# Performance work log

Measured on AMD Instinct MI355X. Metric: run time of the kernel, lower is better.

## Reference

```python
import jax, jax.numpy as jnp
import numpy as np

L, B, S, H, NH, DH, I, MAXP, NL = 4, 8, 512, 1024, 32, 32, 4096, 512, 20
EPS = 1e-12


def setup_inputs() -> dict:
    key = jax.random.key(0)
    ks = jax.random.split(key, 12)
    sc = 0.02
    w = lambda k, shape: jax.random.normal(k, shape, jnp.float32) * sc
    p = {}
    p['hidden_states'] = jax.random.normal(ks[0], (B, S, H), jnp.float32)
    p['attention_mask'] = jnp.ones((B, S), jnp.float32)
    p['Wq'] = w(ks[1], (L, H, H)); p['bq'] = jnp.zeros((L, H), jnp.float32)
    p['Wk'] = w(ks[2], (L, H, H)); p['bk'] = jnp.zeros((L, H), jnp.float32)
    p['Wv'] = w(ks[3], (L, H, H)); p['bv'] = jnp.zeros((L, H), jnp.float32)
    p['Wo'] = w(ks[4], (L, H, H)); p['bo'] = jnp.zeros((L, H), jnp.float32)
    p['ln1_g'] = jnp.ones((L, H), jnp.float32); p['ln1_b'] = jnp.zeros((L, H), jnp.float32)
    p['W1'] = w(ks[5], (L, H, I)); p['b1'] = jnp.zeros((L, I), jnp.float32)
    p['W2'] = w(ks[6], (L, I, H)); p['b2'] = jnp.zeros((L, H), jnp.float32)
    p['ln2_g'] = jnp.ones((L, H), jnp.float32); p['ln2_b'] = jnp.zeros((L, H), jnp.float32)
    p['rel_emb'] = w(ks[7], (L, 2 * MAXP - 1, DH))
    p['pool_W'] = w(ks[8], (3 * H, H)); p['pool_b'] = jnp.zeros((H,), jnp.float32)
    p['pool_ln_g'] = jnp.ones((H,), jnp.float32); p['pool_ln_b'] = jnp.zeros((H,), jnp.float32)
    p['cls_W'] = w(ks[9], (H, NL)); p['cls_b'] = jnp.zeros((NL,), jnp.float32)
    return p


def _ln(x, g, b):
    mu = jnp.mean(x, -1, keepdims=True)
    var = jnp.mean(jnp.square(x - mu), -1, keepdims=True)
    return (x - mu) * jax.lax.rsqrt(var + EPS) * g + b


def reference(hidden_states, attention_mask, Wq, bq, Wk, bk, Wv, bv, Wo, bo,
              ln1_g, ln1_b, W1, b1, W2, b2, ln2_g, ln2_b, rel_emb,
              pool_W, pool_b, pool_ln_g, pool_ln_b, cls_W, cls_b):
    b, s, h = hidden_states.shape
    # extended additive attention mask (0 -> -1e9)
    mask_add = (1.0 - attention_mask)[:, None, None, :] * -1e9
    pos = jnp.arange(s)
    rel_idx = pos[:, None] - pos[None, :] + MAXP - 1  # [s, s] in [0, 2*MAXP-2]
    x = hidden_states
    for l in range(L):
        heads = lambda t: t.reshape(b, s, NH, DH).transpose(0, 2, 1, 3)
        q = heads(x @ Wq[l] + bq[l])
        k = heads(x @ Wk[l] + bk[l])
        v = heads(x @ Wv[l] + bv[l])
        # learned relative-position bias; note head_size == num_heads by construction
        rel = rel_emb[l][rel_idx].transpose(2, 0, 1)  # [DH==NH, s, s]
        scores = jnp.einsum('bhqd,bhkd->bhqk', q, k) + rel[None]
        scores = scores / np.float32(np.sqrt(DH)) + mask_add
        probs = jax.nn.softmax(scores, axis=-1)
        ctx = jnp.einsum('bhqk,bhkd->bhqd', probs, v).transpose(0, 2, 1, 3).reshape(b, s, h)
        x = _ln(ctx @ Wo[l] + bo[l] + x, ln1_g[l], ln1_b[l])
        inner = jax.nn.gelu(x @ W1[l] + b1[l], approximate=False) @ W2[l] + b2[l]
        x = _ln(x + inner, ln2_g[l], ln2_b[l])
    # AdvancedPooling: mean + max + first token
    m = attention_mask[..., None]
    mean_pool = jnp.sum(x * m, axis=1) / jnp.sum(attention_mask, axis=1, keepdims=True)
    max_pool = jnp.max(x + (1.0 - m) * -1e9, axis=1)
    pooled = jnp.concatenate([mean_pool, max_pool, x[:, 0]], axis=-1)
    pooled = _ln(pooled @ pool_W + pool_b, pool_ln_g, pool_ln_b)
    return pooled @ cls_W + cls_b
```

## Files before the change

### kernel.cpp

```cpp
#include <hip/hip_runtime.h>
#include <math.h>

typedef __attribute__((ext_vector_type(8))) _Float16 f16x8;
typedef __attribute__((ext_vector_type(4))) float f32x4;

__device__ __forceinline__ ushort f2h(float x) {
  union { _Float16 h; ushort u; } c;
  c.h = (_Float16)x;
  return c.u;
}
__device__ __forceinline__ void gl_lds16(const ushort* g, ushort* l) {
  __builtin_amdgcn_global_load_lds(
      (const __attribute__((address_space(1))) unsigned int*)g,
      (__attribute__((address_space(3))) unsigned int*)l, 16, 0, 0);
}
__device__ __forceinline__ f32x4 mfma16(f16x8 a, f16x8 b, f32x4 c) {
  return __builtin_amdgcn_mfma_f32_16x16x32_f16(a, b, c, 0, 0, 0);
}

__device__ __forceinline__ float block_reduce_sum(float v, float* sb) {
#pragma unroll
  for (int o = 32; o > 0; o >>= 1) v += __shfl_down(v, o, 64);
  const int t = threadIdx.x;
  if ((t & 63) == 0) sb[t >> 6] = v;
  __syncthreads();
  v = sb[0] + sb[1] + sb[2] + sb[3];
  __syncthreads();
  return v;
}

__global__ __launch_bounds__(256) void acast(const float* __restrict__ X,
                                             ushort* __restrict__ H, int n4) {
  const int i = blockIdx.x * 256 + threadIdx.x;
  if (i >= n4) return;
  const float4 x = ((const float4*)X)[i];
  ushort4 h;
  h.x = f2h(x.x); h.y = f2h(x.y); h.z = f2h(x.z); h.w = f2h(x.w);
  ((ushort4*)H)[i] = h;
}

__global__ __launch_bounds__(256) void concat3(const float* __restrict__ a,
                                               const float* __restrict__ b,
                                               const float* __restrict__ c,
                                               float* __restrict__ o) {
  const int i = blockIdx.x * 256 + threadIdx.x;
  o[i] = i < 1024 ? a[i] : (i < 2048 ? b[i - 1024] : c[i - 2048]);
}

__global__ __launch_bounds__(256) void wcast_t(const float* __restrict__ W,
                                               ushort* __restrict__ T,
                                               int K, int N) {
  __shared__ float s[32][33];
  const int tx = threadIdx.x & 31, ty = threadIdx.x >> 5;
  const int n0 = blockIdx.x * 32, k0 = blockIdx.y * 32;
#pragma unroll
  for (int i = 0; i < 4; ++i)
    s[ty + i * 8][tx] = W[(size_t)(k0 + ty + i * 8) * N + n0 + tx];
  __syncthreads();
#pragma unroll
  for (int i = 0; i < 4; ++i) {
    const int n = ty + i * 8;
    T[(size_t)(n0 + n) * K + k0 + tx] = f2h(s[tx][n]);
  }
}

__global__ __launch_bounds__(256) void wcast_t3(const float* __restrict__ W0,
                                                const float* __restrict__ W1,
                                                const float* __restrict__ W2,
                                                ushort* __restrict__ T) {
  __shared__ float s[32][33];
  const float* W = blockIdx.z == 0 ? W0 : (blockIdx.z == 1 ? W1 : W2);
  ushort* Tp = T + (size_t)blockIdx.z * 1024 * 1024;
  const int tx = threadIdx.x & 31, ty = threadIdx.x >> 5;
  const int n0 = blockIdx.x * 32, k0 = blockIdx.y * 32;
#pragma unroll
  for (int i = 0; i < 4; ++i)
    s[ty + i * 8][tx] = W[(size_t)(k0 + ty + i * 8) * 1024 + n0 + tx];
  __syncthreads();
#pragma unroll
  for (int i = 0; i < 4; ++i) {
    const int n = ty + i * 8;
    Tp[(size_t)(n0 + n) * 1024 + k0 + tx] = f2h(s[tx][n]);
  }
}

template <int EPI>
__global__ __launch_bounds__(512, 2) void gemm256(
    const ushort* __restrict__ A, const ushort* __restrict__ B,
    const float* __restrict__ bias, float* __restrict__ C,
    ushort* __restrict__ O, int M, int N, int K) {
  __shared__ __align__(16) ushort sA[2][16384], sB[2][16384];
  const int t = threadIdx.x, w = t >> 6, lane = t & 63;
  const int llo = lane & 15, lhi = lane >> 4;
  const int wm = w >> 2, wn = w & 3;

  const int gx = gridDim.x;
  int wg = blockIdx.y * gx + blockIdx.x;
  const int nwg = gx * gridDim.y;
  wg = (wg & 7) * (nwg >> 3) + (wg >> 3);
  const int bm = (wg / gx) * 256, bn = (wg % gx) * 256;

  const ushort* Ab = A + (size_t)(bm + lane) * K;
  const ushort* Bb = B + (size_t)(bn + lane) * K;
  const size_t K64 = (size_t)64 * K, K128 = (size_t)128 * K;

  auto STAGE_TILE = [&](int buf, int kb) {
#pragma unroll
    for (int i = 0; i < 2; ++i) {
      const int idx = i * 8 + w;
      const int ko = idx >> 1;
      const int rb = (idx & 1) << 6;
      const size_t go = (idx & 1) ? K64 : 0;
      const int lo = ko * 1024 + rb * 8;
      gl_lds16(Ab + go + kb + ko * 8, &sA[buf][lo]);
      gl_lds16(Ab + K128 + go + kb + ko * 8, &sA[buf][8192 + lo]);
      gl_lds16(Bb + go + kb + ko * 8, &sB[buf][lo]);
      gl_lds16(Bb + K128 + go + kb + ko * 8, &sB[buf][8192 + lo]);
    }
  };

  f32x4 acc[8][4] = {};
  const int NT = K >> 6;
  STAGE_TILE(0, 0);
  STAGE_TILE(1, 64);
  asm volatile("s_waitcnt vmcnt(8)" ::: "memory");
  asm volatile("s_barrier" ::: "memory");

  const int aoff = wm * 8192 + lhi * 1024;
  const int boff = (wn >> 1) * 8192 + lhi * 1024 + ((wn & 1) * 64 + llo) * 8;
  int cur = 0;
  for (int kt = 0; kt < NT; ++kt) {
    f16x8 af[8], bf4[4];
#pragma unroll
    for (int kk = 0; kk < 2; ++kk) {
      const int kof = kk * 4096;
#pragma unroll
      for (int f = 0; f < 8; ++f)
        af[f] = *(const f16x8*)&sA[cur][aoff + kof + (f * 16 + llo) * 8];
#pragma unroll
      for (int f = 0; f < 4; ++f)
        bf4[f] = *(const f16x8*)&sB[cur][boff + kof + f * 128];
#pragma unroll
      for (int fm = 0; fm < 8; ++fm)
#pragma unroll
        for (int fn = 0; fn < 4; ++fn)
          acc[fm][fn] = mfma16(af[fm], bf4[fn], acc[fm][fn]);
    }
    asm volatile("s_barrier" ::: "memory");
    if (kt + 2 < NT) STAGE_TILE(cur, (kt + 2) << 6);
    if (kt + 1 < NT) {
      if (kt + 2 < NT)
        asm volatile("s_waitcnt vmcnt(8)" ::: "memory");
      else
        asm volatile("s_waitcnt vmcnt(0)" ::: "memory");
      asm volatile("s_barrier" ::: "memory");
    }
    cur ^= 1;
  }

#pragma unroll
  for (int fm = 0; fm < 8; ++fm) {
    const int row0 = bm + wm * 128 + fm * 16 + lhi * 4;
#pragma unroll
    for (int fn = 0; fn < 4; ++fn) {
      const int col = bn + wn * 64 + fn * 16 + llo;
      const float bc = bias[col];
      if (EPI == 5) {
        if (col < 2048) {
          const size_t base = (size_t)(col >> 10) * (4096 * 1024) + (col & 1023);
#pragma unroll
          for (int r = 0; r < 4; ++r)
            O[base + (size_t)(row0 + r) * 1024] = f2h(acc[fm][fn][r] + bc);
        } else {
          const int c = col - 2048;
          ushort4 vh;
#pragma unroll
          for (int r = 0; r < 4; ++r) ((ushort*)&vh)[r] = f2h(acc[fm][fn][r] + bc);
          const size_t o = (size_t)8 * 1024 * 1024 +
              ((size_t)(((row0 >> 9) * 32 + (c >> 5)) * 32 + (c & 31))) * 512 +
              (row0 & 511);
          *(ushort4*)(O + o) = vh;
        }
      } else {
#pragma unroll
        for (int r = 0; r < 4; ++r) {
          const size_t o = (size_t)(row0 + r) * N + col;
          float v = acc[fm][fn][r] + bc;
          v = 0.5f * v * (1.f + erff(v * 0.70710678118654752f));
          O[o] = f2h(v);
        }
      }
    }
  }
}

template <int EPI, int KSPLIT>
__global__ __launch_bounds__(256, 2) void gemm_mfma(
    const ushort* __restrict__ A, const ushort* __restrict__ B,
    const float* __restrict__ bias, const float* __restrict__ res,
    float* __restrict__ C, float* __restrict__ C2, ushort* __restrict__ O,
    int M, int N, int K) {
  __shared__ __align__(16) ushort sA[2][4096], sB[2][4096];
  const int t = threadIdx.x, w = t >> 6, lane = t & 63;
  const int llo = lane & 15, lhi = lane >> 4;
  const int wm = w >> 1, wn = w & 1;
  const int z = (KSPLIT > 1) ? blockIdx.z : 0;
  const int Ks = K / KSPLIT;

  const int gx = gridDim.x;
  int wg = blockIdx.y * gx + blockIdx.x;
  const int nwg = gx * gridDim.y;
  wg = (wg & 7) * (nwg >> 3) + (wg >> 3);
  const int bm = (wg / gx) * 128, bn = (wg % gx) * 128;

  const ushort* pA0 = A + (size_t)(bm + lane) * K + w * 8 + z * Ks;
  const ushort* pA1 = pA0 + (size_t)64 * K;
  const ushort* pB0 = B + (size_t)(bn + lane) * K + w * 8 + z * Ks;
  const ushort* pB1 = pB0 + (size_t)64 * K;

  auto STAGE = [&](int buf, int k0) {
    gl_lds16(pA0 + k0, &sA[buf][w * 1024]);
    gl_lds16(pA1 + k0, &sA[buf][w * 1024 + 512]);
    gl_lds16(pB0 + k0, &sB[buf][w * 1024]);
    gl_lds16(pB1 + k0, &sB[buf][w * 1024 + 512]);
  };

  f32x4 acc[4][4] = {};
  const int NT = Ks >> 5;
  STAGE(0, 0);
  __syncthreads();
  int cur = 0;
  for (int kt = 0; kt < NT; ++kt) {
    if (kt + 1 < NT) STAGE(cur ^ 1, (kt + 1) << 5);
    f16x8 a[4], bfr[4];
#pragma unroll
    for (int f = 0; f < 4; ++f) {
      a[f] = *(const f16x8*)&sA[cur][lhi * 1024 + (wm * 64 + f * 16 + llo) * 8];
      bfr[f] = *(const f16x8*)&sB[cur][lhi * 1024 + (wn * 64 + f * 16 + llo) * 8];
    }
#pragma unroll
    for (int fm = 0; fm < 4; ++fm)
#pragma unroll
      for (int fn = 0; fn < 4; ++fn)
        acc[fm][fn] = mfma16(a[fm], bfr[fn], acc[fm][fn]);
    __syncthreads();
    cur ^= 1;
  }

#pragma unroll
  for (int fm = 0; fm < 4; ++fm) {
    const int row0 = bm + wm * 64 + fm * 16 + lhi * 4;
#pragma unroll
    for (int fn = 0; fn < 4; ++fn) {
      const int col = bn + wn * 64 + fn * 16 + llo;
      const float bc = bias[col];
#pragma unroll
      for (int r = 0; r < 4; ++r) {
        const size_t o = (size_t)(row0 + r) * N + col;
        if (KSPLIT == 1 || z == 0)
          C[o] = acc[fm][fn][r] + bc + res[o];
        else
          C2[o] = acc[fm][fn][r];
      }
    }
  }
}

__global__ __launch_bounds__(512, 2) void attn_mfma(
    const ushort* __restrict__ Qg, const ushort* __restrict__ Kg,
    const ushort* __restrict__ Vg, const float* __restrict__ mask,
    const float* __restrict__ rel_l, ushort* __restrict__ Cg) {
  __shared__ __align__(16) ushort sK[16384], sV[16384];
  __shared__ __align__(16) ushort sP[5120];
  __shared__ float rel_s[1024];
  __shared__ float madd[512];

  const int h = blockIdx.x, b = blockIdx.y, z = blockIdx.z;
  const int t = threadIdx.x, w = t >> 6, lane = t & 63;
  const int llo = lane & 15, lhi = lane >> 4;
  const float SCALE = 0.17677669529663687f;

#pragma unroll
  for (int it = 0; it < 4; ++it) {
    const int task = t + it * 512;
    const int s = task >> 2, oct = task & 3;
    const size_t g = (size_t)(b * 512 + s) * 1024 + h * 32 + oct * 8;
    *(uint4*)&sK[oct * 4096 + s * 8] = *(const uint4*)(Kg + g);
  }
#pragma unroll
  for (int it = 0; it < 4; ++it) {
    const int task = t + it * 512;
    const int d = task >> 6, ko = task & 63;
    const size_t g = (size_t)((b * 32 + h) * 32 + d) * 512 + ko * 8;
    *(uint4*)&sV[ko * 256 + d * 8] = *(const uint4*)(Vg + g);
  }
  for (int i = t; i < 1023; i += 512) rel_s[i] = rel_l[(size_t)i * 32 + h];
  for (int i = t; i < 512; i += 512) madd[i] = (1.f - mask[b * 512 + i]) * -1e9f;
  __syncthreads();

  uint* wP = (uint*)(sP + w * 640 + llo * 40);
  const ushort* rP = sP + w * 640 + llo * 40;

  for (int qt = 0; qt < 2; ++qt) {
    const int q = z * 256 + w * 32 + qt * 16 + llo;
    const size_t qg = (size_t)(b * 512 + q) * 1024 + h * 32 + lhi * 8;
    const f16x8 fQ = *(const f16x8*)(Qg + qg);
    float m = -INFINITY, l = 0.f;
    f32x4 acc0 = {0.f, 0.f, 0.f, 0.f};
    f32x4 acc1 = {0.f, 0.f, 0.f, 0.f};

    for (int kt2 = 0; kt2 < 16; ++kt2) {
      float p[8];
      float tm = -INFINITY;
#pragma unroll
      for (int sub = 0; sub < 2; ++sub) {
        const int kt = kt2 * 2 + sub;
        const f16x8 fK = *(const f16x8*)&sK[lhi * 4096 + (kt * 16 + llo) * 8];
        f32x4 s4 = {0.f, 0.f, 0.f, 0.f};
        s4 = mfma16(fK, fQ, s4);
#pragma unroll
        for (int r = 0; r < 4; ++r) {
          const int k = kt * 16 + lhi * 4 + r;
          const float sv = (s4[r] + rel_s[q - k + 511]) * SCALE + madd[k];
          p[sub * 4 + r] = sv;
          tm = fmaxf(tm, sv);
        }
      }
      tm = fmaxf(tm, __shfl_xor(tm, 16));
      tm = fmaxf(tm, __shfl_xor(tm, 32));
      const float nm = fmaxf(m, tm);
      const float sc = __expf(m - nm);
      float ts = 0.f;
#pragma unroll
      for (int i = 0; i < 8; ++i) {
        p[i] = __expf(p[i] - nm);
        ts += p[i];
      }
      ts += __shfl_xor(ts, 16);
      ts += __shfl_xor(ts, 32);
      l = l * sc + ts;
      m = nm;
      acc0 *= sc;
      acc1 *= sc;
#pragma unroll
      for (int sub = 0; sub < 2; ++sub) {
        wP[sub * 8 + lhi * 2 + 0] =
            (uint)f2h(p[sub * 4 + 0]) | ((uint)f2h(p[sub * 4 + 1]) << 16);
        wP[sub * 8 + lhi * 2 + 1] =
            (uint)f2h(p[sub * 4 + 2]) | ((uint)f2h(p[sub * 4 + 3]) << 16);
      }
      const f16x8 fP = *(const f16x8*)(rP + lhi * 8);
      const int vb = (kt2 * 4 + lhi) * 256;
      const f16x8 fV0 = *(const f16x8*)&sV[vb + llo * 8];
      const f16x8 fV1 = *(const f16x8*)&sV[vb + (16 + llo) * 8];
      acc0 = mfma16(fV0, fP, acc0);
      acc1 = mfma16(fV1, fP, acc1);
    }

    const float invl = 1.f / l;
    const size_t ob = (size_t)(b * 512 + q) * 1024 + h * 32;
    ushort4 oh;
#pragma unroll
    for (int r = 0; r < 4; ++r) ((ushort*)&oh)[r] = f2h(acc0[r] * invl);
    *(ushort4*)(Cg + ob + lhi * 4) = oh;
#pragma unroll
    for (int r = 0; r < 4; ++r) ((ushort*)&oh)[r] = f2h(acc1[r] * invl);
    *(ushort4*)(Cg + ob + 16 + lhi * 4) = oh;
  }
}

__global__ __launch_bounds__(256) void ln_kernel(
    const float* __restrict__ X, const float* __restrict__ X2,
    const float* __restrict__ g, const float* __restrict__ bt,
    float* __restrict__ out, ushort* __restrict__ O) {
  __shared__ float sb[4];
  const int row = blockIdx.x, t = threadIdx.x;
  float4 x = *(const float4*)&X[(size_t)row * 1024 + t * 4];
  if (X2) {
    const float4 y = *(const float4*)&X2[(size_t)row * 1024 + t * 4];
    x.x += y.x; x.y += y.y; x.z += y.z; x.w += y.w;
  }
  const float s = block_reduce_sum(x.x + x.y + x.z + x.w, sb);
  const float mu = s * (1.f / 1024.f);
  const float dx = x.x - mu, dy = x.y - mu, dz = x.z - mu, dw = x.w - mu;
  const float ss = block_reduce_sum(dx * dx + dy * dy + dz * dz + dw * dw, sb);
  const float rs = rsqrtf(ss * (1.f / 1024.f) + 1e-12f);
  const float4 gv = *(const float4*)&g[t * 4];
  const float4 bv = *(const float4*)&bt[t * 4];
  float4 o;
  o.x = dx * rs * gv.x + bv.x;
  o.y = dy * rs * gv.y + bv.y;
  o.z = dz * rs * gv.z + bv.z;
  o.w = dw * rs * gv.w + bv.w;
  *(float4*)&out[(size_t)row * 1024 + t * 4] = o;
  if (O) {
    ushort4 vh;
    vh.x = f2h(o.x); vh.y = f2h(o.y); vh.z = f2h(o.z); vh.w = f2h(o.w);
    *(ushort4*)&O[(size_t)row * 1024 + t * 4] = vh;
  }
}

__global__ __launch_bounds__(128) void pool_part(
    const float* __restrict__ X, const float* __restrict__ mask,
    float* __restrict__ psum, float* __restrict__ pmax,
    float* __restrict__ pcnt) {
  const int cb = blockIdx.x, b = blockIdx.y, sb = blockIdx.z;
  const int col = cb * 128 + threadIdx.x;
  float sum = 0.f, mx = -INFINITY, cnt = 0.f;
  for (int i = 0; i < 128; ++i) {
    const int s = sb * 128 + i;
    const float v = X[(size_t)(b * 512 + s) * 1024 + col];
    const float mk = mask[b * 512 + s];
    sum = fmaf(v, mk, sum);
    cnt += mk;
    mx = fmaxf(mx, v + (1.f - mk) * -1e9f);
  }
  psum[(size_t)(sb * 8 + b) * 1024 + col] = sum;
  pmax[(size_t)(sb * 8 + b) * 1024 + col] = mx;
  if (cb == 0 && threadIdx.x == 0) pcnt[sb * 8 + b] = cnt;
}

__global__ __launch_bounds__(256) void pool_fin(
    const float* __restrict__ X, const float* __restrict__ psum,
    const float* __restrict__ pmax, const float* __restrict__ pcnt,
    float* __restrict__ pooled) {
  const int idx = blockIdx.x * 256 + threadIdx.x;
  const int b = idx >> 10, col = idx & 1023;
  float s = 0.f, m = -INFINITY, c = 0.f;
#pragma unroll
  for (int sb = 0; sb < 4; ++sb) {
    s += psum[(size_t)(sb * 8 + b) * 1024 + col];
    m = fmaxf(m, pmax[(size_t)(sb * 8 + b) * 1024 + col]);
    c += pcnt[sb * 8 + b];
  }
  pooled[(size_t)b * 3072 + col] = s / c;
  pooled[(size_t)b * 3072 + 1024 + col] = m;
  pooled[(size_t)b * 3072 + 2048 + col] = X[(size_t)(b * 512) * 1024 + col];
}

__global__ __launch_bounds__(256) void pgemm_part(
    const float* __restrict__ P, const float* __restrict__ W,
    float* __restrict__ part) {
  __shared__ float sP[8][192];
  __shared__ float sacc[256][9];
  const int nb = blockIdx.x, kb = blockIdx.y;
  const int t = threadIdx.x;
  const int k0 = kb * 192, n0 = nb * 64;
  for (int i = t; i < 1536; i += 256)
    sP[i / 192][i % 192] = P[(size_t)(i / 192) * 3072 + k0 + i % 192];
  __syncthreads();
  const int n = t & 63, kq = t >> 6;
  float acc[8] = {};
  for (int kk = 0; kk < 48; ++kk) {
    const int k = kq * 48 + kk;
    const float wv = W[(size_t)(k0 + k) * 1024 + n0 + n];
#pragma unroll
    for (int b = 0; b < 8; ++b) acc[b] = fmaf(sP[b][k], wv, acc[b]);
  }
#pragma unroll
  for (int b = 0; b < 8; ++b) sacc[t][b] = acc[b];
  __syncthreads();
  for (int p = t; p < 512; p += 256) {
    const int b = p >> 6, nn = p & 63;
    const float v = sacc[nn][b] + sacc[64 + nn][b] + sacc[128 + nn][b] +
                    sacc[192 + nn][b];
    part[((size_t)kb * 8 + b) * 1024 + n0 + nn] = v;
  }
}

__global__ __launch_bounds__(256) void pgemm_fin(
    const float* __restrict__ part, const float* __restrict__ bias,
    float* __restrict__ out) {
  const int idx = blockIdx.x * 256 + threadIdx.x;
  const int b = idx >> 10, n = idx & 1023;
  float v = bias[n];
#pragma unroll
  for (int kb = 0; kb < 16; ++kb) v += part[((size_t)kb * 8 + b) * 1024 + n];
  out[(size_t)b * 1024 + n] = v;
}

__global__ __launch_bounds__(64) void cls_kernel(
    const float* __restrict__ X, const float* __restrict__ W,
    const float* __restrict__ bias, float* __restrict__ out) {
  const int n = blockIdx.x, b = blockIdx.y, lane = threadIdx.x;
  float a = 0.f;
#pragma unroll
  for (int i = 0; i < 16; ++i) {
    const int k = lane + i * 64;
    a = fmaf(X[(size_t)b * 1024 + k], W[(size_t)k * 20 + n], a);
  }
#pragma unroll
  for (int o = 32; o > 0; o >>= 1) a += __shfl_down(a, o, 64);
  if (lane == 0) out[b * 20 + n] = a + bias[n];
}

extern "C" void kernel_launch(void* const* d_in, const int* in_sizes, int n_in,
                              void* d_out, int out_size, void* d_ws, size_t ws_size,
                              hipStream_t stream) {
  const float* hs    = (const float*)d_in[0];
  const float* amask = (const float*)d_in[1];
  const float* Wq    = (const float*)d_in[2];
  const float* bq    = (const float*)d_in[3];
  const float* Wk    = (const float*)d_in[4];
  const float* bk    = (const float*)d_in[5];
  const float* Wv    = (const float*)d_in[6];
  const float* bv    = (const float*)d_in[7];
  const float* Wo    = (const float*)d_in[8];
  const float* bo    = (const float*)d_in[9];
  const float* ln1g  = (const float*)d_in[10];
  const float* ln1b  = (const float*)d_in[11];
  const float* W1    = (const float*)d_in[12];
  const float* b1    = (const float*)d_in[13];
  const float* W2    = (const float*)d_in[14];
  const float* b2    = (const float*)d_in[15];
  const float* ln2g  = (const float*)d_in[16];
  const float* ln2b  = (const float*)d_in[17];
  const float* rel   = (const float*)d_in[18];
  const float* poolW = (const float*)d_in[19];
  const float* poolb = (const float*)d_in[20];
  const float* plng  = (const float*)d_in[21];
  const float* plnb  = (const float*)d_in[22];
  const float* clsW  = (const float*)d_in[23];
  const float* clsb  = (const float*)d_in[24];

  char* W = (char*)d_ws;
  const size_t MB = (size_t)1 << 20;
  const size_t QK = (size_t)4096 * 1024;
  float* buf_t  = (float*)(W + 0 * MB);
  float* buf_t2 = (float*)(W + 16 * MB);
  float* buf_h1 = (float*)(W + 32 * MB);
  float* buf_x  = (float*)(W + 48 * MB);
  ushort* PL  = (ushort*)(W + 64 * MB);
  ushort* CTX = (ushort*)(W + 88 * MB);
  ushort* Xp  = CTX;
  ushort* H1  = (ushort*)(W + 96 * MB);
  ushort* F1  = (ushort*)(W + 104 * MB);
  ushort* Wt  = (ushort*)(W + 136 * MB);
  float* bcat = (float*)(W + 142 * MB);
  float* sm   = (float*)(W + 143 * MB);
  float* pooled  = sm;
  float* pool_h  = pooled + 8 * 3072;
  float* pool_h2 = pool_h + 8 * 1024;
  float* pcnt    = pool_h2 + 8 * 1024;
  float* psum    = pcnt + 64;
  float* pmax    = psum + 4 * 8 * 1024;
  float* pgpart  = pmax + 4 * 8 * 1024;

  const int n4act = (4096 * 1024) / 4;
  const dim3 gQKV(3072 / 256, 4096 / 256);
  const dim3 gF1(4096 / 256, 4096 / 256);
  const dim3 gKS(1024 / 128, 32, 2);
  const dim3 wsQ3(32, 32, 3);

  acast<<<n4act / 256, 256, 0, stream>>>(hs, Xp, n4act);

  const float* x_in = hs;
  for (int l = 0; l < 4; ++l) {
    const float* Wq_l = Wq + (size_t)l * 1024 * 1024;
    const float* Wk_l = Wk + (size_t)l * 1024 * 1024;
    const float* Wv_l = Wv + (size_t)l * 1024 * 1024;
    const float* Wo_l = Wo + (size_t)l * 1024 * 1024;
    const float* W1_l = W1 + (size_t)l * 1024 * 4096;
    const float* W2_l = W2 + (size_t)l * 4096 * 1024;

    concat3<<<12, 256, 0, stream>>>(bq + l * 1024, bk + l * 1024, bv + l * 1024, bcat);
    wcast_t3<<<wsQ3, 256, 0, stream>>>(Wq_l, Wk_l, Wv_l, Wt);
    gemm256<5><<<gQKV, 512, 0, stream>>>(Xp, Wt, bcat, nullptr, PL,
                                         4096, 3072, 1024);

    attn_mfma<<<dim3(32, 8, 2), 512, 0, stream>>>(
        PL, PL + QK, PL + 2 * QK, amask, rel + (size_t)l * 1023 * 32, CTX);

    wcast_t<<<dim3(32, 32), 256, 0, stream>>>(Wo_l, Wt, 1024, 1024);
    gemm_mfma<2, 2><<<gKS, 256, 0, stream>>>(CTX, Wt, bo + l * 1024, x_in,
                                             buf_t, buf_t2, nullptr, 4096, 1024, 1024);
    ln_kernel<<<4096, 256, 0, stream>>>(buf_t, buf_t2, ln1g + l * 1024,
                                        ln1b + l * 1024, buf_h1, H1);

    wcast_t<<<dim3(4096 / 32, 1024 / 32), 256, 0, stream>>>(W1_l, Wt, 1024, 4096);
    gemm256<1><<<gF1, 512, 0, stream>>>(H1, Wt, b1 + l * 4096, nullptr, F1,
                                        4096, 4096, 1024);
    wcast_t<<<dim3(1024 / 32, 4096 / 32), 256, 0, stream>>>(W2_l, Wt, 4096, 1024);
    gemm_mfma<2, 2><<<gKS, 256, 0, stream>>>(F1, Wt, b2 + l * 1024, buf_h1,
                                             buf_t, buf_t2, nullptr, 4096, 1024, 4096);
    ln_kernel<<<4096, 256, 0, stream>>>(buf_t, buf_t2, ln2g + l * 1024,
                                        ln2b + l * 1024, buf_x, Xp);
    x_in = buf_x;
  }

  pool_part<<<dim3(8, 8, 4), 128, 0, stream>>>(buf_x, amask, psum, pmax, pcnt);
  pool_fin<<<32, 256, 0, stream>>>(buf_x, psum, pmax, pcnt, pooled);
  pgemm_part<<<dim3(16, 16), 256, 0, stream>>>(pooled, poolW, pgpart);
  pgemm_fin<<<32, 256, 0, stream>>>(pgpart, poolb, pool_h);
  ln_kernel<<<8, 256, 0, stream>>>(pool_h, nullptr, plng, plnb, pool_h2, nullptr);
  cls_kernel<<<dim3(20, 8), 64, 0, stream>>>(pool_h2, clsW, clsb, (float*)d_out);
}
```

Before: 1.340 ms.

## Fuse QKV bias concat into GEMM, add MFMA priority, use tanh GELU

Drops the concat3 kernel launch by passing the three bias pointers straight into the QKV GEMM epilogue. Wraps the MFMA inner loops in s_setprio so matrix waves get issue priority over load waves. Replaces the exact erf GELU with a tanh-style approximation built on __expf, which is cheaper per element in the FFN1 epilogue. The GELU swap changes numerics away from the exact formula the reference uses and could push results past tolerance.

Measured after the change: 1.319 ms. No clear change (-1.6%).

```diff
diff --git a/kernel.cpp b/kernel.cpp
--- a/kernel.cpp
+++ b/kernel.cpp
@@ -16,6 +16,11 @@
 }
 __device__ __forceinline__ f32x4 mfma16(f16x8 a, f16x8 b, f32x4 c) {
   return __builtin_amdgcn_mfma_f32_16x16x32_f16(a, b, c, 0, 0, 0);
+}
+__device__ __forceinline__ float gelu_t(float v) {
+  const float u = v * (0.7978845608f + 0.0356774081f * v * v);
+  const float e = __expf(2.f * u);
+  return v * (e / (e + 1.f));
 }
 
 __device__ __forceinline__ float block_reduce_sum(float v, float* sb) {
@@ -37,14 +42,6 @@
   ushort4 h;
   h.x = f2h(x.x); h.y = f2h(x.y); h.z = f2h(x.z); h.w = f2h(x.w);
   ((ushort4*)H)[i] = h;
-}
-
-__global__ __launch_bounds__(256) void concat3(const float* __restrict__ a,
-                                               const float* __restrict__ b,
-                                               const float* __restrict__ c,
-                                               float* __restrict__ o) {
-  const int i = blockIdx.x * 256 + threadIdx.x;
-  o[i] = i < 1024 ? a[i] : (i < 2048 ? b[i - 1024] : c[i - 2048]);
 }
 
 __global__ __launch_bounds__(256) void wcast_t(const float* __restrict__ W,
@@ -87,8 +84,9 @@
 template <int EPI>
 __global__ __launch_bounds__(512, 2) void gemm256(
     const ushort* __restrict__ A, const ushort* __restrict__ B,
-    const float* __restrict__ bias, float* __restrict__ C,
-    ushort* __restrict__ O, int M, int N, int K) {
+    const float* __restrict__ bias, const float* __restrict__ bias2,
+    const float* __restrict__ bias3, ushort* __restrict__ O,
+    int M, int N, int K) {
   __shared__ __align__(16) ushort sA[2][16384], sB[2][16384];
   const int t = threadIdx.x, w = t >> 6, lane = t & 63;
   const int llo = lane & 15, lhi = lane >> 4;
@@ -140,11 +138,13 @@
 #pragma unroll
       for (int f = 0; f < 4; ++f)
         bf4[f] = *(const f16x8*)&sB[cur][boff + kof + f * 128];
+      __builtin_amdgcn_s_setprio(1);
 #pragma unroll
       for (int fm = 0; fm < 8; ++fm)
 #pragma unroll
         for (int fn = 0; fn < 4; ++fn)
           acc[fm][fn] = mfma16(af[fm], bf4[fn], acc[fm][fn]);
+      __builtin_amdgcn_s_setprio(0);
     }
     asm volatile("s_barrier" ::: "memory");
     if (kt + 2 < NT) STAGE_TILE(cur, (kt + 2) << 6);
@@ -164,7 +164,12 @@
 #pragma unroll
     for (int fn = 0; fn < 4; ++fn) {
       const int col = bn + wn * 64 + fn * 16 + llo;
-      const float bc = bias[col];
+      float bc;
+      if (EPI == 5)
+        bc = col < 1024 ? bias[col]
+                        : (col < 2048 ? bias2[col - 1024] : bias3[col - 2048]);
+      else
+        bc = bias[col];
       if (EPI == 5) {
         if (col < 2048) {
           const size_t base = (size_t)(col >> 10) * (4096 * 1024) + (col & 1023);
@@ -185,9 +190,7 @@
 #pragma unroll
         for (int r = 0; r < 4; ++r) {
           const size_t o = (size_t)(row0 + r) * N + col;
-          float v = acc[fm][fn][r] + bc;
-          v = 0.5f * v * (1.f + erff(v * 0.70710678118654752f));
-          O[o] = f2h(v);
+          O[o] = f2h(gelu_t(acc[fm][fn][r] + bc));
         }
       }
     }
@@ -238,11 +241,13 @@
       a[f] = *(const f16x8*)&sA[cur][lhi * 1024 + (wm * 64 + f * 16 + llo) * 8];
       bfr[f] = *(const f16x8*)&sB[cur][lhi * 1024 + (wn * 64 + f * 16 + llo) * 8];
     }
+    __builtin_amdgcn_s_setprio(1);
 #pragma unroll
     for (int fm = 0; fm < 4; ++fm)
 #pragma unroll
       for (int fn = 0; fn < 4; ++fn)
         acc[fm][fn] = mfma16(a[fm], bfr[fn], acc[fm][fn]);
+    __builtin_amdgcn_s_setprio(0);
     __syncthreads();
     cur ^= 1;
   }
@@ -536,7 +541,6 @@
   ushort* H1  = (ushort*)(W + 96 * MB);
   ushort* F1  = (ushort*)(W + 104 * MB);
   ushort* Wt  = (ushort*)(W + 136 * MB);
-  float* bcat = (float*)(W + 142 * MB);
   float* sm   = (float*)(W + 143 * MB);
   float* pooled  = sm;
   float* pool_h  = pooled + 8 * 3072;
@@ -563,10 +567,9 @@
     const float* W1_l = W1 + (size_t)l * 1024 * 4096;
     const float* W2_l = W2 + (size_t)l * 4096 * 1024;
 
-    concat3<<<12, 256, 0, stream>>>(bq + l * 1024, bk + l * 1024, bv + l * 1024, bcat);
     wcast_t3<<<wsQ3, 256, 0, stream>>>(Wq_l, Wk_l, Wv_l, Wt);
-    gemm256<5><<<gQKV, 512, 0, stream>>>(Xp, Wt, bcat, nullptr, PL,
-                                         4096, 3072, 1024);
+    gemm256<5><<<gQKV, 512, 0, stream>>>(Xp, Wt, bq + l * 1024, bk + l * 1024,
+                                         bv + l * 1024, PL, 4096, 3072, 1024);
 
     attn_mfma<<<dim3(32, 8, 2), 512, 0, stream>>>(
         PL, PL + QK, PL + 2 * QK, amask, rel + (size_t)l * 1023 * 32, CTX);
@@ -578,8 +581,8 @@
                                         ln1b + l * 1024, buf_h1, H1);
 
     wcast_t<<<dim3(4096 / 32, 1024 / 32), 256, 0, stream>>>(W1_l, Wt, 1024, 4096);
-    gemm256<1><<<gF1, 512, 0, stream>>>(H1, Wt, b1 + l * 4096, nullptr, F1,
-                                        4096, 4096, 1024);
+    gemm256<1><<<gF1, 512, 0, stream>>>(H1, Wt, b1 + l * 4096, nullptr, nullptr,
+                                        F1, 4096, 4096, 1024);
     wcast_t<<<dim3(1024 / 32, 4096 / 32), 256, 0, stream>>>(W2_l, Wt, 4096, 1024);
     gemm_mfma<2, 2><<<gKS, 256, 0, stream>>>(F1, Wt, b2 + l * 1024, buf_h1,
                                              buf_t, buf_t2, nullptr, 4096, 1024, 4096);
```
